# Optimization experiments

Hardware: AMD Instinct MI355X
Metric: run time of the kernel (lower is better)

Reference implementation:

```python
import jax, jax.numpy as jnp
import numpy as np

K = 2            # top-k experts
TEMP = 1.0       # temperature
LN_EPS = 1e-5

def setup_inputs() -> dict:
    key = jax.random.key(0)
    B, S, D, E = 4, 4096, 2048, 64
    k0, k1, k2, k3 = jax.random.split(key, 4)
    x = jax.random.normal(k0, (B, S, D), dtype=jnp.float32)
    Wg = jax.random.normal(k1, (E, D), dtype=jnp.float32) * 0.02       # base_gate weight [out,in]
    gamma = jnp.ones((D,), jnp.float32)                                 # LayerNorm weight
    beta = jnp.zeros((D,), jnp.float32)                                 # LayerNorm bias
    W1 = jax.random.normal(k2, (D // 2, D), dtype=jnp.float32) * 0.02   # diff_pred linear1
    W2 = jax.random.normal(k3, (1, D // 2), dtype=jnp.float32) * 0.02   # diff_pred linear2
    return {"x": x, "Wg": Wg, "gamma": gamma, "beta": beta, "W1": W1, "W2": W2}

def reference(x, Wg, gamma, beta, W1, W2):
    # base expert logits: [B,S,E]
    logits = jnp.einsum('bsd,ed->bse', x, Wg)
    # difficulty predictor: LN -> Linear -> GELU -> Linear -> sigmoid, [B,S,1]
    mu = jnp.mean(x, axis=-1, keepdims=True)
    var = jnp.var(x, axis=-1, keepdims=True)
    h = (x - mu) * jax.lax.rsqrt(var + LN_EPS) * gamma + beta
    h1 = jax.nn.gelu(jnp.einsum('bsd,hd->bsh', h, W1), approximate=False)
    diff = jax.nn.sigmoid(jnp.einsum('bsh,oh->bso', h1, W2))
    # modulate + temperature (eval mode: no jitter / mask_drop)
    logits = logits / (1.0 + diff) * (1.0 / TEMP)
    probs_soft = jax.nn.softmax(logits, axis=-1)
    # top-k selection
    _, idx = jax.lax.top_k(logits, K)                    # [B,S,K]
    hard_any = jnp.max(jax.nn.one_hot(idx, logits.shape[-1], dtype=probs_soft.dtype), axis=2)  # [B,S,E]
    probs_st = hard_any - probs_soft + probs_soft        # faithful to source (no detach)
    scores = jnp.take_along_axis(probs_st, idx, axis=-1)  # [B,S,K]
    scores = scores / jnp.maximum(jnp.sum(scores, axis=-1, keepdims=True), 1e-9)
    importance = jax.lax.stop_gradient(jnp.mean(probs_soft, axis=(0, 1)))  # [E]
    load = jax.lax.stop_gradient(jnp.mean(hard_any, axis=(0, 1)))          # [E]
    return (idx, scores, probs_soft, importance, load)
```

## Files before the change

### kernel.cpp

```cpp
#include <hip/hip_runtime.h>
#include <math.h>

#define BS_TOK 16384
#define DIM    2048
#define NEXP   64
#define DHID   1024
#define GKS    4
#define KSL    (DIM / GKS)

typedef __attribute__((ext_vector_type(8))) _Float16 f16x8;
typedef __attribute__((ext_vector_type(4))) float    f32x4;

#define GLOBAL_AS const __attribute__((address_space(1))) void*
#define LDS_AS    __attribute__((address_space(3))) void*
#define GLDS16(g, l) __builtin_amdgcn_global_load_lds((GLOBAL_AS)(g), (LDS_AS)(l), 16, 0, 0)

__device__ __forceinline__ float gelu_f(float x) {
  return 0.5f * x * (1.0f + erff(x * 0.70710678118654752440f));
}

#define GATE_NB 1024
#define LN_NB   4096
#define CAST_NB 1024

__global__ __launch_bounds__(256) void prep_kernel(const float* __restrict__ X,
                                                   const float* __restrict__ Wg,
                                                   const float* __restrict__ gamma,
                                                   const float* __restrict__ beta,
                                                   const float* __restrict__ W1,
                                                   _Float16* __restrict__ H,
                                                   _Float16* __restrict__ W1h,
                                                   float* __restrict__ logitsP) {
  const int bid = blockIdx.x;
  const int tid = threadIdx.x;
  __shared__ float sX[16][68];
  __shared__ float sW[16][68];

  if (bid < GATE_NB) {
    const int m0   = (bid >> 2) * 64;
    const int k0   = (bid & 3) * KSL;
    const int srow = tid >> 2;
    const int skq  = tid & 3;
    const int ty   = tid >> 4;
    const int tx   = tid & 15;
    const float* xb = X  + (size_t)(m0 + srow) * DIM + k0 + skq * 4;
    const float* wb = Wg + (size_t)srow * DIM + k0 + skq * 4;
    float acc[4][4] = {};
    float4 rx = *(const float4*)xb;
    float4 rw = *(const float4*)wb;
    for (int kt = 0; kt < KSL; kt += 16) {
      __syncthreads();
      sX[skq * 4 + 0][srow] = rx.x;
      sX[skq * 4 + 1][srow] = rx.y;
      sX[skq * 4 + 2][srow] = rx.z;
      sX[skq * 4 + 3][srow] = rx.w;
      sW[skq * 4 + 0][srow] = rw.x;
      sW[skq * 4 + 1][srow] = rw.y;
      sW[skq * 4 + 2][srow] = rw.z;
      sW[skq * 4 + 3][srow] = rw.w;
      const int ktn = (kt + 16 < KSL) ? kt + 16 : 0;
      rx = *(const float4*)(xb + ktn);
      rw = *(const float4*)(wb + ktn);
      __syncthreads();
#pragma unroll
      for (int k = 0; k < 16; ++k) {
        const float4 a4 = *(const float4*)&sX[k][ty * 4];
        const float4 b4 = *(const float4*)&sW[k][tx * 4];
        const float av[4] = {a4.x, a4.y, a4.z, a4.w};
        const float bv[4] = {b4.x, b4.y, b4.z, b4.w};
#pragma unroll
        for (int i = 0; i < 4; ++i)
#pragma unroll
          for (int j = 0; j < 4; ++j) acc[i][j] += av[i] * bv[j];
      }
    }
    float* op = logitsP + (size_t)(bid & 3) * (BS_TOK * NEXP)
              + (size_t)(m0 + ty * 4) * NEXP + tx * 4;
#pragma unroll
    for (int i = 0; i < 4; ++i) {
      float4 o;
      o.x = acc[i][0]; o.y = acc[i][1]; o.z = acc[i][2]; o.w = acc[i][3];
      *(float4*)(op + (size_t)i * NEXP) = o;
    }
  } else if (bid < GATE_NB + LN_NB) {
    const int w    = tid >> 6, lane = tid & 63;
    const int t    = (bid - GATE_NB) * 4 + w;
    const float* xr = X + (size_t)t * DIM;
    float4 xv[8];
#pragma unroll
    for (int j = 0; j < 4; ++j) {
      const int c0 = (j * 64 + lane) * 8;
      xv[j * 2]     = *(const float4*)(xr + c0);
      xv[j * 2 + 1] = *(const float4*)(xr + c0 + 4);
    }
    float s = 0.f, q = 0.f;
#pragma unroll
    for (int j = 0; j < 8; ++j) {
      s += (xv[j].x + xv[j].y) + (xv[j].z + xv[j].w);
      q += (xv[j].x * xv[j].x + xv[j].y * xv[j].y) + (xv[j].z * xv[j].z + xv[j].w * xv[j].w);
    }
#pragma unroll
    for (int off = 32; off > 0; off >>= 1) {
      s += __shfl_xor(s, off);
      q += __shfl_xor(q, off);
    }
    const float mu  = s * (1.0f / DIM);
    const float var = q * (1.0f / DIM) - mu * mu;
    const float rs  = rsqrtf(var + 1e-5f);
#pragma unroll
    for (int j = 0; j < 4; ++j) {
      const int c0 = (j * 64 + lane) * 8;
      const float4 g0 = *(const float4*)(gamma + c0);
      const float4 g1 = *(const float4*)(gamma + c0 + 4);
      const float4 b0 = *(const float4*)(beta + c0);
      const float4 b1 = *(const float4*)(beta + c0 + 4);
      const float4 a = xv[j * 2], b = xv[j * 2 + 1];
      f16x8 h;
      h[0] = (_Float16)((a.x - mu) * rs * g0.x + b0.x);
      h[1] = (_Float16)((a.y - mu) * rs * g0.y + b0.y);
      h[2] = (_Float16)((a.z - mu) * rs * g0.z + b0.z);
      h[3] = (_Float16)((a.w - mu) * rs * g0.w + b0.w);
      h[4] = (_Float16)((b.x - mu) * rs * g1.x + b1.x);
      h[5] = (_Float16)((b.y - mu) * rs * g1.y + b1.y);
      h[6] = (_Float16)((b.z - mu) * rs * g1.z + b1.z);
      h[7] = (_Float16)((b.w - mu) * rs * g1.w + b1.w);
      *(f16x8*)(H + (size_t)t * DIM + c0) = h;
    }
  } else {
    const int i = ((bid - GATE_NB - LN_NB) * 256 + tid) * 8;
    const float4 a = *(const float4*)(W1 + i);
    const float4 b = *(const float4*)(W1 + i + 4);
    f16x8 o;
    o[0] = (_Float16)a.x; o[1] = (_Float16)a.y; o[2] = (_Float16)a.z; o[3] = (_Float16)a.w;
    o[4] = (_Float16)b.x; o[5] = (_Float16)b.y; o[6] = (_Float16)b.z; o[7] = (_Float16)b.w;
    *(f16x8*)(W1h + i) = o;
  }
}

__global__ __launch_bounds__(256) void g2_kernel(const _Float16* __restrict__ H,
                                                 const _Float16* __restrict__ W1h,
                                                 const float* __restrict__ W2,
                                                 float* __restrict__ diffz) {
  __shared__ __align__(16) _Float16 sA[2][4096];
  __shared__ __align__(16) _Float16 sB[2][4096];
  const int bid = blockIdx.x;
  const int c   = bid & 7;
  const int j   = bid >> 3;
  const int m0  = (c * 16 + (j >> 3)) * 128;
  const int n0  = (j & 7) * 128;
  const int tid  = threadIdx.x;
  const int w    = tid >> 6, lane = tid & 63;
  const int wr   = w >> 1,  wc   = w & 1;
  const int col  = lane & 15, quad = lane >> 4;
  const int r    = lane & 15, q = lane >> 4;
  const int gA   = w * 2;
  const _Float16* srcA0 = H   + (size_t)(m0 + gA * 16 + r) * DIM + q * 8;
  const _Float16* srcA1 = srcA0 + (size_t)16 * DIM;
  const _Float16* srcB0 = W1h + (size_t)(n0 + gA * 16 + r) * DIM + q * 8;
  const _Float16* srcB1 = srcB0 + (size_t)16 * DIM;
  const int dOff = gA * 512 + lane * 8;
  f32x4 acc[4][4] = {};
  GLDS16(srcA0, &sA[0][dOff]);
  GLDS16(srcA1, &sA[0][dOff + 512]);
  GLDS16(srcB0, &sB[0][dOff]);
  GLDS16(srcB1, &sB[0][dOff + 512]);
  for (int it = 0; it < 64; ++it) {
    const int cb = it & 1;
    __syncthreads();
    if (it < 63) {
      const int kt2 = (it + 1) << 5;
      const int nb  = cb ^ 1;
      GLDS16(srcA0 + kt2, &sA[nb][dOff]);
      GLDS16(srcA1 + kt2, &sA[nb][dOff + 512]);
      GLDS16(srcB0 + kt2, &sB[nb][dOff]);
      GLDS16(srcB1 + kt2, &sB[nb][dOff + 512]);
    }
    f16x8 af[4], bf[4];
#pragma unroll
    for (int mi = 0; mi < 4; ++mi)
      af[mi] = *(const f16x8*)&sA[cb][(wr * 4 + mi) * 512 + lane * 8];
#pragma unroll
    for (int ni = 0; ni < 4; ++ni)
      bf[ni] = *(const f16x8*)&sB[cb][(wc * 4 + ni) * 512 + lane * 8];
#pragma unroll
    for (int mi = 0; mi < 4; ++mi)
#pragma unroll
      for (int ni = 0; ni < 4; ++ni)
        acc[mi][ni] = __builtin_amdgcn_mfma_f32_16x16x32_f16(af[mi], bf[ni], acc[mi][ni], 0, 0, 0);
  }
  float w2v[4];
#pragma unroll
  for (int ni = 0; ni < 4; ++ni) w2v[ni] = W2[n0 + wc * 64 + ni * 16 + col];
#pragma unroll
  for (int mi = 0; mi < 4; ++mi) {
#pragma unroll
    for (int reg = 0; reg < 4; ++reg) {
      float v = 0.f;
#pragma unroll
      for (int ni = 0; ni < 4; ++ni) v += gelu_f(acc[mi][ni][reg]) * w2v[ni];
      v += __shfl_xor(v, 1);
      v += __shfl_xor(v, 2);
      v += __shfl_xor(v, 4);
      v += __shfl_xor(v, 8);
      if (col == 0)
        atomicAdd(diffz + m0 + wr * 64 + mi * 16 + quad * 4 + reg, v);
    }
  }
}

__global__ __launch_bounds__(256) void finalize_kernel(const float* __restrict__ logitsP,
                                                       const float* __restrict__ diffz,
                                                       float* __restrict__ out_idx,
                                                       float* __restrict__ out_scores,
                                                       float* __restrict__ out_probs,
                                                       float* __restrict__ out_imp,
                                                       float* __restrict__ out_load) {
  const int tid  = threadIdx.x;
  const int w    = tid >> 6, lane = tid & 63;
  const size_t PS = (size_t)BS_TOK * NEXP;
  float acc_imp = 0.f, acc_load = 0.f;
  for (int it = 0; it < 8; ++it) {
    const int t    = blockIdx.x * 32 + it * 4 + w;
    const float* lp = logitsP + (size_t)t * NEXP + lane;
    const float L  = ((lp[0] + lp[PS]) + lp[2 * PS]) + lp[3 * PS];
    const float z  = diffz[t];
    const float d  = 1.0f / (1.0f + expf(-z));
    const float l  = L / (1.0f + d);
    float v1 = l; int i1 = lane;
    float v2 = -INFINITY; int i2 = 0;
#pragma unroll
    for (int off = 32; off > 0; off >>= 1) {
      const float ov1 = __shfl_xor(v1, off); const int oi1 = __shfl_xor(i1, off);
      const float ov2 = __shfl_xor(v2, off); const int oi2 = __shfl_xor(i2, off);
      const bool bwin = (ov1 > v1) || (ov1 == v1 && oi1 < i1);
      const float w1 = bwin ? ov1 : v1; const int wi1 = bwin ? oi1 : i1;
      const float l1 = bwin ? v1 : ov1; const int li1 = bwin ? i1 : oi1;
      const float c2 = bwin ? ov2 : v2; const int ci2 = bwin ? oi2 : i2;
      const bool s2w = (c2 > l1) || (c2 == l1 && ci2 < li1);
      v2 = s2w ? c2 : l1; i2 = s2w ? ci2 : li1;
      v1 = w1; i1 = wi1;
    }
    float p = expf(l - v1);
    float s = p;
#pragma unroll
    for (int off = 32; off > 0; off >>= 1) s += __shfl_xor(s, off);
    p /= s;
    const float p1 = __shfl(p, i1);
    const float p2 = __shfl(p, i2);
    const float s1 = (1.0f - p1) + p1;
    const float s2 = (1.0f - p2) + p2;
    const float den = fmaxf(s1 + s2, 1e-9f);
    if (lane == 0) {
      out_idx[t * 2]        = (float)i1;
      out_idx[t * 2 + 1]    = (float)i2;
      out_scores[t * 2]     = s1 / den;
      out_scores[t * 2 + 1] = s2 / den;
    }
    out_probs[(size_t)t * NEXP + lane] = p;
    acc_imp  += p;
    acc_load += (lane == i1 || lane == i2) ? 1.0f : 0.0f;
  }
  __shared__ float s_imp[256];
  __shared__ float s_hard[256];
  s_imp[tid]  = acc_imp;
  s_hard[tid] = acc_load;
  __syncthreads();
  if (tid < 64) {
    const float inv = 1.0f / (float)BS_TOK;
    const float si = s_imp[tid] + s_imp[64 + tid] + s_imp[128 + tid] + s_imp[192 + tid];
    const float sl = s_hard[tid] + s_hard[64 + tid] + s_hard[128 + tid] + s_hard[192 + tid];
    atomicAdd(out_imp + tid, si * inv);
    atomicAdd(out_load + tid, sl * inv);
  }
}

extern "C" void kernel_launch(void* const* d_in, const int* in_sizes, int n_in,
                              void* d_out, int out_size, void* d_ws, size_t ws_size,
                              hipStream_t stream) {
  (void)in_sizes; (void)n_in; (void)out_size; (void)ws_size;
  const float* X     = (const float*)d_in[0];
  const float* Wg    = (const float*)d_in[1];
  const float* gamma = (const float*)d_in[2];
  const float* beta  = (const float*)d_in[3];
  const float* W1    = (const float*)d_in[4];
  const float* W2    = (const float*)d_in[5];
  float* out = (float*)d_out;

  char* ws = (char*)d_ws;
  _Float16* H       = (_Float16*)(ws);
  _Float16* W1h     = (_Float16*)(ws + 67108864ull);
  float*    logitsP = (float*)  (ws + 71303168ull);
  float*    diffz   = (float*)  (ws + 88080384ull);

  float* out_idx    = out;
  float* out_scores = out + 32768;
  float* out_probs  = out + 65536;
  float* out_imp    = out + 1114112;
  float* out_load   = out + 1114176;

  hipMemsetAsync(diffz, 0, 65536ull, stream);
  hipMemsetAsync(out_imp, 0, 512ull, stream);
  prep_kernel<<<GATE_NB + LN_NB + CAST_NB, 256, 0, stream>>>(X, Wg, gamma, beta, W1,
                                                             H, W1h, logitsP);
  g2_kernel<<<(DHID / 128) * (BS_TOK / 128), 256, 0, stream>>>(H, W1h, W2, diffz);
  finalize_kernel<<<BS_TOK / 32, 256, 0, stream>>>(logitsP, diffz, out_idx, out_scores,
                                                   out_probs, out_imp, out_load);
}
```

Baseline: 445.0 us.

## Enlarge gate GEMM tiles, interleave prep roles, and single-buffer K=64 MFMA stages

The gate GEMM now computes 256-token tiles with an 8x8 register tile per thread, which cuts redundant Wg loads and block count. Prep blocks are interleaved by role (1 gate, 16 LayerNorm, 4 cast per group of 21) so the different workloads mix across CUs instead of running in phases. The hidden-layer GEMM drops register-free double buffering for a synchronous load of a 64-wide K slab per iteration, with an occupancy hint of 3 blocks. This risks exposing load latency in g2, since loads no longer overlap compute within a block, and the larger gate tile raises register pressure.

```diff
diff --git a/kernel.cpp b/kernel.cpp
--- a/kernel.cpp
+++ b/kernel.cpp
@@ -19,72 +19,84 @@
   return 0.5f * x * (1.0f + erff(x * 0.70710678118654752440f));
 }
 
-#define GATE_NB 1024
-#define LN_NB   4096
-#define CAST_NB 1024
-
-__global__ __launch_bounds__(256) void prep_kernel(const float* __restrict__ X,
-                                                   const float* __restrict__ Wg,
-                                                   const float* __restrict__ gamma,
-                                                   const float* __restrict__ beta,
-                                                   const float* __restrict__ W1,
-                                                   _Float16* __restrict__ H,
-                                                   _Float16* __restrict__ W1h,
-                                                   float* __restrict__ logitsP) {
-  const int bid = blockIdx.x;
-  const int tid = threadIdx.x;
-  __shared__ float sX[16][68];
+#define PREP_NB (21 * 256)
+
+__global__ __launch_bounds__(256, 2) void prep_kernel(const float* __restrict__ X,
+                                                      const float* __restrict__ Wg,
+                                                      const float* __restrict__ gamma,
+                                                      const float* __restrict__ beta,
+                                                      const float* __restrict__ W1,
+                                                      _Float16* __restrict__ H,
+                                                      _Float16* __restrict__ W1h,
+                                                      float* __restrict__ logitsP) {
+  const int bid  = blockIdx.x;
+  const int tid  = threadIdx.x;
+  const int role = bid % 21;
+  const int grp  = bid / 21;
+  __shared__ float sX[16][264];
   __shared__ float sW[16][68];
 
-  if (bid < GATE_NB) {
-    const int m0   = (bid >> 2) * 64;
-    const int k0   = (bid & 3) * KSL;
+  if (role == 0) {
+    const int gi   = grp;
+    const int m0   = (gi >> 2) * 256;
+    const int ks   = gi & 3;
+    const int k0   = ks * KSL;
     const int srow = tid >> 2;
     const int skq  = tid & 3;
-    const int ty   = tid >> 4;
-    const int tx   = tid & 15;
+    const int tr   = tid >> 3;
+    const int tc   = tid & 7;
     const float* xb = X  + (size_t)(m0 + srow) * DIM + k0 + skq * 4;
     const float* wb = Wg + (size_t)srow * DIM + k0 + skq * 4;
-    float acc[4][4] = {};
-    float4 rx = *(const float4*)xb;
-    float4 rw = *(const float4*)wb;
+    float acc[8][8] = {};
+    float4 rx[4], rw;
+#pragma unroll
+    for (int r = 0; r < 4; ++r) rx[r] = *(const float4*)(xb + (size_t)r * 64 * DIM);
+    rw = *(const float4*)wb;
     for (int kt = 0; kt < KSL; kt += 16) {
       __syncthreads();
-      sX[skq * 4 + 0][srow] = rx.x;
-      sX[skq * 4 + 1][srow] = rx.y;
-      sX[skq * 4 + 2][srow] = rx.z;
-      sX[skq * 4 + 3][srow] = rx.w;
+#pragma unroll
+      for (int r = 0; r < 4; ++r) {
+        sX[skq * 4 + 0][r * 64 + srow] = rx[r].x;
+        sX[skq * 4 + 1][r * 64 + srow] = rx[r].y;
+        sX[skq * 4 + 2][r * 64 + srow] = rx[r].z;
+        sX[skq * 4 + 3][r * 64 + srow] = rx[r].w;
+      }
       sW[skq * 4 + 0][srow] = rw.x;
       sW[skq * 4 + 1][srow] = rw.y;
       sW[skq * 4 + 2][srow] = rw.z;
       sW[skq * 4 + 3][srow] = rw.w;
       const int ktn = (kt + 16 < KSL) ? kt + 16 : 0;
-      rx = *(const float4*)(xb + ktn);
+#pragma unroll
+      for (int r = 0; r < 4; ++r) rx[r] = *(const float4*)(xb + (size_t)r * 64 * DIM + ktn);
       rw = *(const float4*)(wb + ktn);
       __syncthreads();
 #pragma unroll
       for (int k = 0; k < 16; ++k) {
-        const float4 a4 = *(const float4*)&sX[k][ty * 4];
-        const float4 b4 = *(const float4*)&sW[k][tx * 4];
-        const float av[4] = {a4.x, a4.y, a4.z, a4.w};
-        const float bv[4] = {b4.x, b4.y, b4.z, b4.w};
-#pragma unroll
-        for (int i = 0; i < 4; ++i)
-#pragma unroll
-          for (int j = 0; j < 4; ++j) acc[i][j] += av[i] * bv[j];
+        float av[8], bv[8];
+        *(float4*)(av)     = *(const float4*)&sX[k][tr * 8];
+        *(float4*)(av + 4) = *(const float4*)&sX[k][tr * 8 + 4];
+        *(float4*)(bv)     = *(const float4*)&sW[k][tc * 8];
+        *(float4*)(bv + 4) = *(const float4*)&sW[k][tc * 8 + 4];
+#pragma unroll
+        for (int i = 0; i < 8; ++i)
+#pragma unroll
+          for (int j = 0; j < 8; ++j) acc[i][j] += av[i] * bv[j];
       }
     }
-    float* op = logitsP + (size_t)(bid & 3) * (BS_TOK * NEXP)
-              + (size_t)(m0 + ty * 4) * NEXP + tx * 4;
-#pragma unroll
-    for (int i = 0; i < 4; ++i) {
-      float4 o;
-      o.x = acc[i][0]; o.y = acc[i][1]; o.z = acc[i][2]; o.w = acc[i][3];
-      *(float4*)(op + (size_t)i * NEXP) = o;
-    }
-  } else if (bid < GATE_NB + LN_NB) {
+    float* op = logitsP + (size_t)ks * (BS_TOK * NEXP)
+              + (size_t)(m0 + tr * 8) * NEXP + tc * 8;
+#pragma unroll
+    for (int i = 0; i < 8; ++i) {
+      float4 o0, o1;
+      o0.x = acc[i][0]; o0.y = acc[i][1]; o0.z = acc[i][2]; o0.w = acc[i][3];
+      o1.x = acc[i][4]; o1.y = acc[i][5]; o1.z = acc[i][6]; o1.w = acc[i][7];
+      *(float4*)(op + (size_t)i * NEXP)     = o0;
+      *(float4*)(op + (size_t)i * NEXP + 4) = o1;
+    }
+  } else if (role <= 16) {
+    const int lid  = grp * 16 + (role - 1);
     const int w    = tid >> 6, lane = tid & 63;
-    const int t    = (bid - GATE_NB) * 4 + w;
+    const int t    = lid * 4 + w;
     const float* xr = X + (size_t)t * DIM;
     float4 xv[8];
 #pragma unroll
@@ -127,7 +139,8 @@
       *(f16x8*)(H + (size_t)t * DIM + c0) = h;
     }
   } else {
-    const int i = ((bid - GATE_NB - LN_NB) * 256 + tid) * 8;
+    const int cid = grp * 4 + (role - 17);
+    const int i   = (cid * 256 + tid) * 8;
     const float4 a = *(const float4*)(W1 + i);
     const float4 b = *(const float4*)(W1 + i + 4);
     f16x8 o;
@@ -137,12 +150,12 @@
   }
 }
 
-__global__ __launch_bounds__(256) void g2_kernel(const _Float16* __restrict__ H,
-                                                 const _Float16* __restrict__ W1h,
-                                                 const float* __restrict__ W2,
-                                                 float* __restrict__ diffz) {
-  __shared__ __align__(16) _Float16 sA[2][4096];
-  __shared__ __align__(16) _Float16 sB[2][4096];
+__global__ __launch_bounds__(256, 3) void g2_kernel(const _Float16* __restrict__ H,
+                                                    const _Float16* __restrict__ W1h,
+                                                    const float* __restrict__ W2,
+                                                    float* __restrict__ diffz) {
+  __shared__ __align__(16) _Float16 sA[8192];
+  __shared__ __align__(16) _Float16 sB[8192];
   const int bid = blockIdx.x;
   const int c   = bid & 7;
   const int j   = bid >> 3;
@@ -160,33 +173,33 @@
   const _Float16* srcB1 = srcB0 + (size_t)16 * DIM;
   const int dOff = gA * 512 + lane * 8;
   f32x4 acc[4][4] = {};
-  GLDS16(srcA0, &sA[0][dOff]);
-  GLDS16(srcA1, &sA[0][dOff + 512]);
-  GLDS16(srcB0, &sB[0][dOff]);
-  GLDS16(srcB1, &sB[0][dOff + 512]);
-  for (int it = 0; it < 64; ++it) {
-    const int cb = it & 1;
+  for (int kt = 0; kt < DIM; kt += 64) {
     __syncthreads();
-    if (it < 63) {
-      const int kt2 = (it + 1) << 5;
-      const int nb  = cb ^ 1;
-      GLDS16(srcA0 + kt2, &sA[nb][dOff]);
-      GLDS16(srcA1 + kt2, &sA[nb][dOff + 512]);
-      GLDS16(srcB0 + kt2, &sB[nb][dOff]);
-      GLDS16(srcB1 + kt2, &sB[nb][dOff + 512]);
-    }
-    f16x8 af[4], bf[4];
-#pragma unroll
-    for (int mi = 0; mi < 4; ++mi)
-      af[mi] = *(const f16x8*)&sA[cb][(wr * 4 + mi) * 512 + lane * 8];
-#pragma unroll
-    for (int ni = 0; ni < 4; ++ni)
-      bf[ni] = *(const f16x8*)&sB[cb][(wc * 4 + ni) * 512 + lane * 8];
-#pragma unroll
-    for (int mi = 0; mi < 4; ++mi)
+    GLDS16(srcA0 + kt,      sA + dOff);
+    GLDS16(srcA1 + kt,      sA + dOff + 512);
+    GLDS16(srcA0 + kt + 32, sA + 4096 + dOff);
+    GLDS16(srcA1 + kt + 32, sA + 4096 + dOff + 512);
+    GLDS16(srcB0 + kt,      sB + dOff);
+    GLDS16(srcB1 + kt,      sB + dOff + 512);
+    GLDS16(srcB0 + kt + 32, sB + 4096 + dOff);
+    GLDS16(srcB1 + kt + 32, sB + 4096 + dOff + 512);
+    __syncthreads();
+#pragma unroll
+    for (int s = 0; s < 2; ++s) {
+      const int base = s * 4096;
+      f16x8 af[4], bf[4];
+#pragma unroll
+      for (int mi = 0; mi < 4; ++mi)
+        af[mi] = *(const f16x8*)(sA + base + (wr * 4 + mi) * 512 + lane * 8);
 #pragma unroll
       for (int ni = 0; ni < 4; ++ni)
-        acc[mi][ni] = __builtin_amdgcn_mfma_f32_16x16x32_f16(af[mi], bf[ni], acc[mi][ni], 0, 0, 0);
+        bf[ni] = *(const f16x8*)(sB + base + (wc * 4 + ni) * 512 + lane * 8);
+#pragma unroll
+      for (int mi = 0; mi < 4; ++mi)
+#pragma unroll
+        for (int ni = 0; ni < 4; ++ni)
+          acc[mi][ni] = __builtin_amdgcn_mfma_f32_16x16x32_f16(af[mi], bf[ni], acc[mi][ni], 0, 0, 0);
+    }
   }
   float w2v[4];
 #pragma unroll
@@ -300,8 +313,7 @@
 
   hipMemsetAsync(diffz, 0, 65536ull, stream);
   hipMemsetAsync(out_imp, 0, 512ull, stream);
-  prep_kernel<<<GATE_NB + LN_NB + CAST_NB, 256, 0, stream>>>(X, Wg, gamma, beta, W1,
-                                                             H, W1h, logitsP);
+  prep_kernel<<<PREP_NB, 256, 0, stream>>>(X, Wg, gamma, beta, W1, H, W1h, logitsP);
   g2_kernel<<<(DHID / 128) * (BS_TOK / 128), 256, 0, stream>>>(H, W1h, W2, diffz);
   finalize_kernel<<<BS_TOK / 32, 256, 0, stream>>>(logitsP, diffz, out_idx, out_scores,
                                                    out_probs, out_imp, out_load);
```

Result: slower. 480.1 us (+7.9%).
